# Performance work log

Measured on AMD Instinct MI355X. Metric: run time of the kernel, lower is better.

Reference implementation:

```python
import jax, jax.numpy as jnp
import numpy as np

N = 32768      # total points (multiple of patch_size -> no padding needed)
C = 768        # channels
H = 8          # num heads
K = 256        # patch_size (window length)
HD = C // H    # head dim = 96, divisible by 6 (3 axes * rotary pairs)
FREQ = 100.0   # rope_freq


def rope3d(x, pos):
    """Point-position RoPE: head dim split into 3 axis chunks, each rotated
    by angles pos_axis * freq**(-i/half).  x: [N,H,HD], pos: [N,3] float."""
    d_axis = HD // 3            # 32
    half = d_axis // 2          # 16
    inv_freq = FREQ ** (-jnp.arange(half, dtype=x.dtype) / half)   # [half]
    ang = pos[:, :, None] * inv_freq[None, None, :]                # [N,3,half]
    cos = jnp.cos(ang)[:, None, :, :]                              # [N,1,3,half]
    sin = jnp.sin(ang)[:, None, :, :]
    xr = x.reshape(x.shape[0], x.shape[1], 3, d_axis)              # [N,H,3,d_axis]
    x1, x2 = xr[..., :half], xr[..., half:]
    out = jnp.concatenate([x1 * cos - x2 * sin, x1 * sin + x2 * cos], axis=-1)
    return out.reshape(x.shape)


def setup_inputs() -> dict:
    key = jax.random.key(0)
    ks = jax.random.split(key, 6)
    feat = jax.random.normal(ks[0], (N, C), dtype=jnp.float32)
    grid_coord = jax.random.randint(ks[1], (N, 3), 0, 1024, dtype=jnp.int32)
    order = jax.random.permutation(ks[2], N).astype(jnp.int32)     # serialized order
    inverse = jnp.argsort(order).astype(jnp.int32)                 # its inverse
    w_qkv = jax.random.normal(ks[3], (C, 3 * C), dtype=jnp.float32) * 0.02
    b_qkv = jnp.zeros((3 * C,), dtype=jnp.float32)
    w_proj = jax.random.normal(ks[4], (C, C), dtype=jnp.float32) * 0.02
    b_proj = jnp.zeros((C,), dtype=jnp.float32)
    return {"feat": feat, "grid_coord": grid_coord, "order": order,
            "inverse": inverse, "w_qkv": w_qkv, "b_qkv": b_qkv,
            "w_proj": w_proj, "b_proj": b_proj}


def reference(feat, grid_coord, order, inverse, w_qkv, b_qkv, w_proj, b_proj):
    scale = HD ** -0.5
    P = N // K  # number of windows
    qkv = (feat @ w_qkv + b_qkv)[order]                   # gather by serialized order
    pos = grid_coord[order].astype(feat.dtype)            # [N,3]
    q, k, v = jnp.split(qkv, 3, axis=-1)
    q = rope3d(q.reshape(N, H, HD), pos)
    k = rope3d(k.reshape(N, H, HD), pos)
    v = v.reshape(N, H, HD)
    # windowed (varlen with equal patch lengths) attention
    qw = q.reshape(P, K, H, HD)
    kw = k.reshape(P, K, H, HD)
    vw = v.reshape(P, K, H, HD)
    logits = jnp.einsum('pqhd,pkhd->phqk', qw, kw) * scale
    attn = jax.nn.softmax(logits, axis=-1)
    out = jnp.einsum('phqk,pkhd->pqhd', attn, vw).reshape(N, C)
    out = out[inverse]                                    # scatter back to input order
    return out @ w_proj + b_proj
```

## Files before the change

kernel.cpp:

```cpp
#include <hip/hip_runtime.h>
#include <hip/hip_bf16.h>
#include <stdint.h>

typedef __bf16 bf16_t;
typedef __bf16 bf16x8 __attribute__((ext_vector_type(8)));
typedef __bf16 bf16x4 __attribute__((ext_vector_type(4)));
typedef float f32x4 __attribute__((ext_vector_type(4)));

template <int V> struct ic { static constexpr int value = V; };

__device__ __forceinline__ void gload_lds16(const bf16_t* g, bf16_t* l) {
  __builtin_amdgcn_global_load_lds((const __attribute__((address_space(1))) void*)g,
                                   (__attribute__((address_space(3))) void*)l, 16, 0, 0);
}

__global__ __launch_bounds__(256) void transpose_cast_k(const float* __restrict__ W,
                                                        bf16_t* __restrict__ Bt,
                                                        int KDin, int MDin) {
  __shared__ float tile[64][65];
  const int bm = blockIdx.x, bk = blockIdx.y;
  const int c = threadIdx.x & 63, r0 = threadIdx.x >> 6;
#pragma unroll
  for (int rr = 0; rr < 16; ++rr) {
    int row = rr * 4 + r0;
    tile[row][c] = W[(size_t)(bk * 64 + row) * MDin + bm * 64 + c];
  }
  __syncthreads();
#pragma unroll
  for (int rr = 0; rr < 16; ++rr) {
    int mo = rr * 4 + r0;
    Bt[(size_t)(bm * 64 + mo) * KDin + bk * 64 + c] = (bf16_t)tile[c][mo];
  }
}

__global__ __launch_bounds__(256) void gather_cast_k(const float* __restrict__ feat,
                                                     const int* __restrict__ order,
                                                     const int* __restrict__ grid_coord,
                                                     bf16_t* __restrict__ featp,
                                                     float* __restrict__ posf) {
  const int id = blockIdx.x * 256 + threadIdx.x;
  const int j = id / 192;
  const int c = (id % 192) * 4;
  const int g = order[j];
  const float4 v = *(const float4*)(feat + (size_t)g * 768 + c);
  bf16x4 o;
  o[0] = (bf16_t)v.x; o[1] = (bf16_t)v.y; o[2] = (bf16_t)v.z; o[3] = (bf16_t)v.w;
  *(bf16x4*)(featp + (size_t)j * 768 + c) = o;
  if (c == 0) {
    posf[j * 3 + 0] = (float)grid_coord[g * 3 + 0];
    posf[j * 3 + 1] = (float)grid_coord[g * 3 + 1];
    posf[j * 3 + 2] = (float)grid_coord[g * 3 + 2];
  }
}

template <int MODE, int NBX>
__global__ __launch_bounds__(512, 2) void gemm256_k(const bf16_t* __restrict__ A,
                                                    const bf16_t* __restrict__ Bt,
                                                    const float* __restrict__ bias,
                                                    bf16_t* __restrict__ Cq,
                                                    bf16_t* __restrict__ Ck,
                                                    bf16_t* __restrict__ Cv,
                                                    float* __restrict__ Cf,
                                                    const int* __restrict__ order,
                                                    const float* __restrict__ posf) {
  extern __shared__ bf16_t sm[];
  bf16_t* ldsA = sm;
  bf16_t* ldsB = sm + 4 * 8192;

  const int tid = threadIdx.x;
  const int lane = tid & 63, wave = tid >> 6;
  const int wr = wave >> 2, wc = wave & 3;
  const int lq = lane & 15, lk = lane >> 4;

  const int bid = blockIdx.x;
  const int cpx = gridDim.x >> 3;
  const int rm = (bid & 7) * cpx + (bid >> 3);
  const int by = rm / NBX, bx = rm % NBX;

  const int o0 = tid, o1 = tid + 512;
  const int r0s = o0 >> 2, ls0 = (o0 & 3) ^ ((r0s >> 1) & 3);
  const int r1s = o1 >> 2, ls1 = (o1 & 3) ^ ((r1s >> 1) & 3);
  const bf16_t* pA0 = A + (size_t)(by * 256 + r0s) * 768 + ls0 * 8;
  const bf16_t* pA1 = A + (size_t)(by * 256 + r1s) * 768 + ls1 * 8;
  const bf16_t* pB0 = Bt + (size_t)(bx * 256 + r0s) * 768 + ls0 * 8;
  const bf16_t* pB1 = Bt + (size_t)(bx * 256 + r1s) * 768 + ls1 * 8;

  auto stageA = [&](int kt) {
    bf16_t* d = ldsA + ((kt & 3) << 13);
    gload_lds16(pA0 + kt * 32, d + o0 * 8);
    gload_lds16(pA1 + kt * 32, d + o1 * 8);
  };
  auto stageB = [&](int kt) {
    bf16_t* d = ldsB + ((kt & 3) << 13);
    gload_lds16(pB0 + kt * 32, d + o0 * 8);
    gload_lds16(pB1 + kt * 32, d + o1 * 8);
  };

  const int pslot = lk ^ ((lq >> 1) & 3);

  f32x4 acc[8][4] = {};

  stageA(0); stageB(0); stageA(1); stageB(1); stageA(2); stageB(2);
  asm volatile("s_waitcnt vmcnt(8)" ::: "memory");
  __builtin_amdgcn_s_barrier();
  __builtin_amdgcn_sched_barrier(0);

  auto group = [&](int t, auto VMC, auto STGC) {
    constexpr int VM = decltype(VMC)::value;
    constexpr bool STG = decltype(STGC)::value;
    const bf16_t* Ab = ldsA + ((t & 3) << 13);
    const bf16_t* Bb = ldsB + ((t & 3) << 13);
    bf16x8 af[4], bfr[4];
#pragma unroll
    for (int m = 0; m < 4; ++m)
      af[m] = *(const bf16x8*)(Ab + (wr * 128 + m * 16 + lq) * 32 + pslot * 8);
#pragma unroll
    for (int n = 0; n < 4; ++n)
      bfr[n] = *(const bf16x8*)(Bb + (wc * 64 + n * 16 + lq) * 32 + pslot * 8);
    if constexpr (STG) stageA(t + 3);
    __builtin_amdgcn_s_barrier();
    asm volatile("s_waitcnt lgkmcnt(0)" ::: "memory");
    __builtin_amdgcn_s_setprio(1);
#pragma unroll
    for (int n = 0; n < 4; ++n)
#pragma unroll
      for (int m = 0; m < 4; ++m)
        acc[m][n] = __builtin_amdgcn_mfma_f32_16x16x32_bf16(af[m], bfr[n], acc[m][n], 0, 0, 0);
    __builtin_amdgcn_s_setprio(0);
    __builtin_amdgcn_s_barrier();
#pragma unroll
    for (int m = 0; m < 4; ++m)
      af[m] = *(const bf16x8*)(Ab + (wr * 128 + 64 + m * 16 + lq) * 32 + pslot * 8);
    if constexpr (STG) stageB(t + 3);
    if constexpr (VM == 8) asm volatile("s_waitcnt vmcnt(8)" ::: "memory");
    else if constexpr (VM == 4) asm volatile("s_waitcnt vmcnt(4)" ::: "memory");
    else if constexpr (VM == 0) asm volatile("s_waitcnt vmcnt(0)" ::: "memory");
    __builtin_amdgcn_s_barrier();
    asm volatile("s_waitcnt lgkmcnt(0)" ::: "memory");
    __builtin_amdgcn_s_setprio(1);
#pragma unroll
    for (int n = 0; n < 4; ++n)
#pragma unroll
      for (int m = 0; m < 4; ++m)
        acc[4 + m][n] = __builtin_amdgcn_mfma_f32_16x16x32_bf16(af[m], bfr[n], acc[4 + m][n], 0, 0, 0);
    __builtin_amdgcn_s_setprio(0);
    __builtin_amdgcn_s_barrier();
    __builtin_amdgcn_sched_barrier(0);
  };

  for (int t = 0; t < 21; ++t) group(t, ic<8>{}, ic<1>{});
  group(21, ic<4>{}, ic<0>{});
  group(22, ic<0>{}, ic<0>{});
  group(23, ic<-1>{}, ic<0>{});

  const int colb = bx * 256 + wc * 64;
  float bcol[4];
#pragma unroll
  for (int n = 0; n < 4; ++n) bcol[n] = bias[colb + n * 16 + lq];

  if (MODE == 0) {
    const int sec = bx / 3;
    bf16_t* base = sec == 0 ? Cq : (sec == 1 ? Ck : Cv);
    const int coll = colb - sec * 768;
    if (sec < 2) {
      const int a0 = (colb % 96) >> 5;
      const int a1 = ((colb + 32) % 96) >> 5;
      const float fr = exp2f(-0.41524101186f * (float)lq);
#pragma unroll
      for (int m = 0; m < 8; ++m) {
        const int rowb = by * 256 + wr * 128 + m * 16 + lk * 4;
#pragma unroll
        for (int r = 0; r < 4; ++r) {
          const int row = rowb + r;
          float s0, c0, s1, c1;
          __sincosf(posf[row * 3 + a0] * fr, &s0, &c0);
          __sincosf(posf[row * 3 + a1] * fr, &s1, &c1);
          const float x1 = acc[m][0][r] + bcol[0], x2 = acc[m][1][r] + bcol[1];
          const float y1 = acc[m][2][r] + bcol[2], y2 = acc[m][3][r] + bcol[3];
          acc[m][0][r] = x1 * c0 - x2 * s0;
          acc[m][1][r] = x1 * s0 + x2 * c0;
          acc[m][2][r] = y1 * c1 - y2 * s1;
          acc[m][3][r] = y1 * s1 + y2 * c1;
        }
#pragma unroll
        for (int n = 0; n < 4; ++n) {
          const int col = coll + n * 16 + lq;
#pragma unroll
          for (int r = 0; r < 4; ++r)
            base[(size_t)(rowb + r) * 768 + col] = (bf16_t)acc[m][n][r];
        }
      }
    } else {
#pragma unroll
      for (int m = 0; m < 8; ++m) {
        const int rowb = by * 256 + wr * 128 + m * 16 + lk * 4;
#pragma unroll
        for (int n = 0; n < 4; ++n) {
          const int col = coll + n * 16 + lq;
#pragma unroll
          for (int r = 0; r < 4; ++r)
            base[(size_t)(rowb + r) * 768 + col] = (bf16_t)(acc[m][n][r] + bcol[n]);
        }
      }
    }
  } else {
#pragma unroll
    for (int m = 0; m < 8; ++m) {
      const int rowb = by * 256 + wr * 128 + m * 16 + lk * 4;
      int ro[4];
#pragma unroll
      for (int r = 0; r < 4; ++r) ro[r] = order[rowb + r];
#pragma unroll
      for (int n = 0; n < 4; ++n) {
        const int col = colb + n * 16 + lq;
#pragma unroll
        for (int r = 0; r < 4; ++r)
          Cf[(size_t)ro[r] * 768 + col] = acc[m][n][r] + bcol[n];
      }
    }
  }
}

__global__ __launch_bounds__(256) void pack_k(const bf16_t* __restrict__ Kb,
                                              const bf16_t* __restrict__ Vb,
                                              bf16_t* __restrict__ Kp,
                                              bf16_t* __restrict__ Vp) {
  __shared__ bf16_t VT[96 * 264];
  const int h = blockIdx.x, p = blockIdx.y;
  const int tid = threadIdx.x;
  const int tok0 = p * 256;
  const size_t phb = (size_t)(p * 8 + h) * 24576;

#pragma unroll
  for (int i = 0; i < 12; ++i) {
    const int c = i * 256 + tid;
    const int fi = c >> 6, ln = c & 63;
    const int nt = fi / 3, a = fi - nt * 3;
    const int tok = nt * 16 + (ln & 15), feat = a * 32 + (ln >> 4) * 8;
    *(bf16x8*)(Kp + phb + (size_t)c * 8) =
        *(const bf16x8*)(Kb + (size_t)(tok0 + tok) * 768 + h * 96 + feat);
  }

  {
    const bf16_t* vrow = Vb + (size_t)(tok0 + tid) * 768 + h * 96;
#pragma unroll
    for (int d0 = 0; d0 < 96; d0 += 8) {
      bf16x8 v = *(const bf16x8*)(vrow + d0);
#pragma unroll
      for (int i = 0; i < 8; ++i) VT[(d0 + i) * 264 + tid] = v[i];
    }
  }
  __syncthreads();
#pragma unroll
  for (int i = 0; i < 12; ++i) {
    const int c = i * 256 + tid;
    const int fi = c >> 6, ln = c & 63;
    const int d = (fi >> 3) * 16 + (ln & 15);
    const int tb = (fi & 7) * 32 + (ln >> 4) * 8;
    *(bf16x8*)(Vp + phb + (size_t)c * 8) = *(const bf16x8*)(VT + d * 264 + tb);
  }
}

__global__ __launch_bounds__(256) void attn_k(bf16_t* QO,
                                              const bf16_t* __restrict__ Kp,
                                              const bf16_t* __restrict__ Vp) {
  __shared__ bf16_t KV[24576];
  __shared__ bf16_t Pb[4][2048];
  const int bid = blockIdx.x;
  const int chunk = bid & 3;
  const int ph = bid >> 2;
  const int h = ph & 7, p = ph >> 3;
  const int tid = threadIdx.x, lane = tid & 63, wave = tid >> 6;
  const int lq = lane & 15, lk = lane >> 4;
  const int tok0 = p * 256;
  const int qrow0 = chunk * 64 + wave * 16;
  const bf16_t* Kps = Kp + (size_t)ph * 24576;
  const bf16_t* Vps = Vp + (size_t)ph * 24576;
  const float scale = 0.10206207262f;

#pragma unroll
  for (int i = 0; i < 12; ++i)
    gload_lds16(Kps + i * 2048 + tid * 8, KV + i * 2048 + tid * 8);
  bf16x8 aq[3];
  {
    const bf16_t* qb = QO + (size_t)(tok0 + qrow0 + lq) * 768 + h * 96 + lk * 8;
#pragma unroll
    for (int kc = 0; kc < 3; ++kc) aq[kc] = *(const bf16x8*)(qb + kc * 32);
  }
  __syncthreads();

  f32x4 sacc[16];
#pragma unroll
  for (int nt = 0; nt < 16; ++nt) {
    f32x4 acc = {0.f, 0.f, 0.f, 0.f};
#pragma unroll
    for (int kc = 0; kc < 3; ++kc) {
      bf16x8 bk = *(const bf16x8*)(KV + (size_t)((nt * 3 + kc) * 64 + lane) * 8);
      acc = __builtin_amdgcn_mfma_f32_16x16x32_bf16(aq[kc], bk, acc, 0, 0, 0);
    }
    sacc[nt] = acc;
  }
  __syncthreads();

#pragma unroll
  for (int i = 0; i < 12; ++i)
    gload_lds16(Vps + i * 2048 + tid * 8, KV + i * 2048 + tid * 8);

  float linv[4];
#pragma unroll
  for (int r = 0; r < 4; ++r) {
    float mx = -1e30f;
#pragma unroll
    for (int nt = 0; nt < 16; ++nt) mx = fmaxf(mx, sacc[nt][r]);
    mx = fmaxf(mx, __shfl_xor(mx, 1));
    mx = fmaxf(mx, __shfl_xor(mx, 2));
    mx = fmaxf(mx, __shfl_xor(mx, 4));
    mx = fmaxf(mx, __shfl_xor(mx, 8));
    mx *= scale;
    float l = 0.f;
#pragma unroll
    for (int nt = 0; nt < 16; ++nt) {
      float e = __expf(sacc[nt][r] * scale - mx);
      sacc[nt][r] = e;
      l += e;
    }
    l += __shfl_xor(l, 1);
    l += __shfl_xor(l, 2);
    l += __shfl_xor(l, 4);
    l += __shfl_xor(l, 8);
    linv[r] = 1.f / l;
  }
  __syncthreads();

  bf16_t* pw = &Pb[wave][0];
  f32x4 oacc[6] = {};
#pragma unroll
  for (int hf = 0; hf < 2; ++hf) {
#pragma unroll
    for (int ntl = 0; ntl < 8; ++ntl) {
      const int nt = hf * 8 + ntl;
      const int chk = ntl * 2 + (lq >> 3);
#pragma unroll
      for (int r = 0; r < 4; ++r) {
        const int row = lk * 4 + r;
        const int phys = chk ^ (row & 7);
        pw[row * 128 + phys * 8 + (lq & 7)] = (bf16_t)sacc[nt][r];
      }
    }
#pragma unroll
    for (int kcl = 0; kcl < 4; ++kcl) {
      const int physr = (kcl * 4 + lk) ^ (lq & 7);
      bf16x8 pf = *(const bf16x8*)(pw + lq * 128 + physr * 8);
      const int kc = hf * 4 + kcl;
#pragma unroll
      for (int dt = 0; dt < 6; ++dt) {
        bf16x8 vb = *(const bf16x8*)(KV + (size_t)((dt * 8 + kc) * 64 + lane) * 8);
        oacc[dt] = __builtin_amdgcn_mfma_f32_16x16x32_bf16(pf, vb, oacc[dt], 0, 0, 0);
      }
    }
  }

#pragma unroll
  for (int dt = 0; dt < 6; ++dt) {
#pragma unroll
    for (int r = 0; r < 4; ++r) {
      const int row = tok0 + qrow0 + lk * 4 + r;
      QO[(size_t)row * 768 + h * 96 + dt * 16 + lq] = (bf16_t)(oacc[dt][r] * linv[r]);
    }
  }
}

extern "C" void kernel_launch(void* const* d_in, const int* in_sizes, int n_in,
                              void* d_out, int out_size, void* d_ws, size_t ws_size,
                              hipStream_t stream) {
  const float* feat       = (const float*)d_in[0];
  const int*   grid_coord = (const int*)d_in[1];
  const int*   order      = (const int*)d_in[2];
  const float* w_qkv      = (const float*)d_in[4];
  const float* b_qkv      = (const float*)d_in[5];
  const float* w_proj     = (const float*)d_in[6];
  const float* b_proj     = (const float*)d_in[7];
  float* out = (float*)d_out;

  char* ws = (char*)d_ws;
  bf16_t* Bt1   = (bf16_t*)(ws);
  bf16_t* Bt2   = (bf16_t*)(ws + 3538944);
  bf16_t* featp = (bf16_t*)(ws + 4718592);
  bf16_t* Kp    = featp;
  bf16_t* Qb    = (bf16_t*)(ws + 55050240);
  bf16_t* Kb    = (bf16_t*)(ws + 105381888);
  bf16_t* Vb    = (bf16_t*)(ws + 155713536);
  bf16_t* Vp    = (bf16_t*)(ws + 206045184);
  float*  posf  = (float*)(ws + 206045184);

  static bool attr_set = false;
  if (!attr_set) {
    (void)hipFuncSetAttribute((const void*)gemm256_k<0, 9>,
                              hipFuncAttributeMaxDynamicSharedMemorySize, 131072);
    (void)hipFuncSetAttribute((const void*)gemm256_k<1, 3>,
                              hipFuncAttributeMaxDynamicSharedMemorySize, 131072);
    attr_set = true;
  }

  transpose_cast_k<<<dim3(36, 12), 256, 0, stream>>>(w_qkv, Bt1, 768, 2304);
  transpose_cast_k<<<dim3(12, 12), 256, 0, stream>>>(w_proj, Bt2, 768, 768);
  gather_cast_k<<<24576, 256, 0, stream>>>(feat, order, grid_coord, featp, posf);
  gemm256_k<0, 9><<<1152, 512, 131072, stream>>>(featp, Bt1, b_qkv, Qb, Kb, Vb,
                                                 nullptr, nullptr, posf);
  pack_k<<<dim3(8, 128), 256, 0, stream>>>(Kb, Vb, Kp, Vp);
  attn_k<<<4096, 256, 0, stream>>>(Qb, Kp, Vp);
  gemm256_k<1, 3><<<384, 512, 131072, stream>>>(Qb, Bt2, b_proj, nullptr, nullptr,
                                                nullptr, out, order, nullptr);
}
```

Before: 502.8 us.

## Make GEMMs persistent over 128-row strips looping across all column tiles

Replaces the 256x256-tile GEMM grid with 256 blocks, each owning a 128-row strip of A and looping over every 256-wide column tile. The prefetch for the next tile's B is issued during the last k-steps of the current tile so the pipeline runs without draining. LDS use drops to 96KB and A is re-read from L2 per tile. The intent is to remove the tail-wave imbalance of 1152 and 384 tile launches on a 256-CU device and to overlap tile transitions. In exchange each block does a serial loop over 9 or 3 tiles, and the 128x256 tile has lower arithmetic intensity per LDS load.

```diff
diff --git a/kernel.cpp b/kernel.cpp
--- a/kernel.cpp
+++ b/kernel.cpp
@@ -53,8 +53,8 @@
   }
 }
 
-template <int MODE, int NBX>
-__global__ __launch_bounds__(512, 2) void gemm256_k(const bf16_t* __restrict__ A,
+template <int MODE, int NT>
+__global__ __launch_bounds__(512, 2) void gemm128_k(const bf16_t* __restrict__ A,
                                                     const bf16_t* __restrict__ Bt,
                                                     const float* __restrict__ bias,
                                                     bf16_t* __restrict__ Cq,
@@ -65,61 +65,56 @@
                                                     const float* __restrict__ posf) {
   extern __shared__ bf16_t sm[];
   bf16_t* ldsA = sm;
-  bf16_t* ldsB = sm + 4 * 8192;
+  bf16_t* ldsB = sm + 16384;
 
   const int tid = threadIdx.x;
   const int lane = tid & 63, wave = tid >> 6;
   const int wr = wave >> 2, wc = wave & 3;
   const int lq = lane & 15, lk = lane >> 4;
-
-  const int bid = blockIdx.x;
-  const int cpx = gridDim.x >> 3;
-  const int rm = (bid & 7) * cpx + (bid >> 3);
-  const int by = rm / NBX, bx = rm % NBX;
-
-  const int o0 = tid, o1 = tid + 512;
-  const int r0s = o0 >> 2, ls0 = (o0 & 3) ^ ((r0s >> 1) & 3);
-  const int r1s = o1 >> 2, ls1 = (o1 & 3) ^ ((r1s >> 1) & 3);
-  const bf16_t* pA0 = A + (size_t)(by * 256 + r0s) * 768 + ls0 * 8;
-  const bf16_t* pA1 = A + (size_t)(by * 256 + r1s) * 768 + ls1 * 8;
-  const bf16_t* pB0 = Bt + (size_t)(bx * 256 + r0s) * 768 + ls0 * 8;
-  const bf16_t* pB1 = Bt + (size_t)(bx * 256 + r1s) * 768 + ls1 * 8;
-
-  auto stageA = [&](int kt) {
-    bf16_t* d = ldsA + ((kt & 3) << 13);
-    gload_lds16(pA0 + kt * 32, d + o0 * 8);
-    gload_lds16(pA1 + kt * 32, d + o1 * 8);
+  const int by = blockIdx.x;
+
+  const int oA = tid;
+  const int rA = oA >> 2, lsA = (oA & 3) ^ ((rA >> 1) & 3);
+  const int oB0 = tid, oB1 = tid + 512;
+  const int rB0 = oB0 >> 2, lsB0 = (oB0 & 3) ^ ((rB0 >> 1) & 3);
+  const int rB1 = oB1 >> 2, lsB1 = (oB1 & 3) ^ ((rB1 >> 1) & 3);
+
+  const bf16_t* pA = A + (size_t)(by * 128 + rA) * 768 + lsA * 8;
+  const bf16_t* pB0 = Bt + (size_t)rB0 * 768 + lsB0 * 8;
+  const bf16_t* pB1 = Bt + (size_t)rB1 * 768 + lsB1 * 8;
+
+  auto stage = [&](const bf16_t* sB0, const bf16_t* sB1, int kt, int slot) {
+    bf16_t* dA = ldsA + (slot << 12);
+    bf16_t* dB = ldsB + (slot << 13);
+    gload_lds16(pA + kt * 32, dA + oA * 8);
+    gload_lds16(sB0 + kt * 32, dB + oB0 * 8);
+    gload_lds16(sB1 + kt * 32, dB + oB1 * 8);
   };
-  auto stageB = [&](int kt) {
-    bf16_t* d = ldsB + ((kt & 3) << 13);
-    gload_lds16(pB0 + kt * 32, d + o0 * 8);
-    gload_lds16(pB1 + kt * 32, d + o1 * 8);
-  };
 
   const int pslot = lk ^ ((lq >> 1) & 3);
 
-  f32x4 acc[8][4] = {};
-
-  stageA(0); stageB(0); stageA(1); stageB(1); stageA(2); stageB(2);
-  asm volatile("s_waitcnt vmcnt(8)" ::: "memory");
-  __builtin_amdgcn_s_barrier();
-  __builtin_amdgcn_sched_barrier(0);
-
-  auto group = [&](int t, auto VMC, auto STGC) {
+  f32x4 acc[4][4];
+
+  auto ph = [&](int t, const bf16_t* sB0, const bf16_t* sB1, int skt,
+                auto VMC, auto STGC) {
     constexpr int VM = decltype(VMC)::value;
     constexpr bool STG = decltype(STGC)::value;
-    const bf16_t* Ab = ldsA + ((t & 3) << 13);
+    const bf16_t* Ab = ldsA + ((t & 3) << 12);
     const bf16_t* Bb = ldsB + ((t & 3) << 13);
     bf16x8 af[4], bfr[4];
 #pragma unroll
     for (int m = 0; m < 4; ++m)
-      af[m] = *(const bf16x8*)(Ab + (wr * 128 + m * 16 + lq) * 32 + pslot * 8);
+      af[m] = *(const bf16x8*)(Ab + (wr * 64 + m * 16 + lq) * 32 + pslot * 8);
 #pragma unroll
     for (int n = 0; n < 4; ++n)
       bfr[n] = *(const bf16x8*)(Bb + (wc * 64 + n * 16 + lq) * 32 + pslot * 8);
-    if constexpr (STG) stageA(t + 3);
+    if constexpr (STG) stage(sB0, sB1, skt, (t + 3) & 3);
+    if constexpr (VM == 6) asm volatile("s_waitcnt vmcnt(6)" ::: "memory");
+    else if constexpr (VM == 3) asm volatile("s_waitcnt vmcnt(3)" ::: "memory");
+    else if constexpr (VM == 0) asm volatile("s_waitcnt vmcnt(0)" ::: "memory");
     __builtin_amdgcn_s_barrier();
     asm volatile("s_waitcnt lgkmcnt(0)" ::: "memory");
+    __builtin_amdgcn_sched_barrier(0);
     __builtin_amdgcn_s_setprio(1);
 #pragma unroll
     for (int n = 0; n < 4; ++n)
@@ -128,96 +123,106 @@
         acc[m][n] = __builtin_amdgcn_mfma_f32_16x16x32_bf16(af[m], bfr[n], acc[m][n], 0, 0, 0);
     __builtin_amdgcn_s_setprio(0);
     __builtin_amdgcn_s_barrier();
-#pragma unroll
-    for (int m = 0; m < 4; ++m)
-      af[m] = *(const bf16x8*)(Ab + (wr * 128 + 64 + m * 16 + lq) * 32 + pslot * 8);
-    if constexpr (STG) stageB(t + 3);
-    if constexpr (VM == 8) asm volatile("s_waitcnt vmcnt(8)" ::: "memory");
-    else if constexpr (VM == 4) asm volatile("s_waitcnt vmcnt(4)" ::: "memory");
-    else if constexpr (VM == 0) asm volatile("s_waitcnt vmcnt(0)" ::: "memory");
-    __builtin_amdgcn_s_barrier();
-    asm volatile("s_waitcnt lgkmcnt(0)" ::: "memory");
-    __builtin_amdgcn_s_setprio(1);
-#pragma unroll
-    for (int n = 0; n < 4; ++n)
-#pragma unroll
-      for (int m = 0; m < 4; ++m)
-        acc[4 + m][n] = __builtin_amdgcn_mfma_f32_16x16x32_bf16(af[m], bfr[n], acc[4 + m][n], 0, 0, 0);
-    __builtin_amdgcn_s_setprio(0);
-    __builtin_amdgcn_s_barrier();
     __builtin_amdgcn_sched_barrier(0);
   };
 
-  for (int t = 0; t < 21; ++t) group(t, ic<8>{}, ic<1>{});
-  group(21, ic<4>{}, ic<0>{});
-  group(22, ic<0>{}, ic<0>{});
-  group(23, ic<-1>{}, ic<0>{});
-
-  const int colb = bx * 256 + wc * 64;
-  float bcol[4];
-#pragma unroll
-  for (int n = 0; n < 4; ++n) bcol[n] = bias[colb + n * 16 + lq];
-
-  if (MODE == 0) {
-    const int sec = bx / 3;
-    bf16_t* base = sec == 0 ? Cq : (sec == 1 ? Ck : Cv);
-    const int coll = colb - sec * 768;
-    if (sec < 2) {
-      const int a0 = (colb % 96) >> 5;
-      const int a1 = ((colb + 32) % 96) >> 5;
-      const float fr = exp2f(-0.41524101186f * (float)lq);
-#pragma unroll
-      for (int m = 0; m < 8; ++m) {
-        const int rowb = by * 256 + wr * 128 + m * 16 + lk * 4;
-#pragma unroll
-        for (int r = 0; r < 4; ++r) {
-          const int row = rowb + r;
-          float s0, c0, s1, c1;
-          __sincosf(posf[row * 3 + a0] * fr, &s0, &c0);
-          __sincosf(posf[row * 3 + a1] * fr, &s1, &c1);
-          const float x1 = acc[m][0][r] + bcol[0], x2 = acc[m][1][r] + bcol[1];
-          const float y1 = acc[m][2][r] + bcol[2], y2 = acc[m][3][r] + bcol[3];
-          acc[m][0][r] = x1 * c0 - x2 * s0;
-          acc[m][1][r] = x1 * s0 + x2 * c0;
-          acc[m][2][r] = y1 * c1 - y2 * s1;
-          acc[m][3][r] = y1 * s1 + y2 * c1;
+  stage(pB0, pB1, 0, 0);
+  stage(pB0, pB1, 1, 1);
+  stage(pB0, pB1, 2, 2);
+  asm volatile("s_waitcnt vmcnt(6)" ::: "memory");
+  __builtin_amdgcn_s_barrier();
+  __builtin_amdgcn_sched_barrier(0);
+
+  for (int tile = 0; tile < NT; ++tile) {
+#pragma unroll
+    for (int m = 0; m < 4; ++m)
+#pragma unroll
+      for (int n = 0; n < 4; ++n) acc[m][n] = f32x4{0.f, 0.f, 0.f, 0.f};
+
+    const bf16_t* nB0 = pB0 + 256 * 768;
+    const bf16_t* nB1 = pB1 + 256 * 768;
+
+    for (int t = 0; t < 21; ++t) ph(t, pB0, pB1, t + 3, ic<6>{}, ic<1>{});
+    if (tile < NT - 1) {
+      ph(21, nB0, nB1, 0, ic<6>{}, ic<1>{});
+      ph(22, nB0, nB1, 1, ic<6>{}, ic<1>{});
+      ph(23, nB0, nB1, 2, ic<6>{}, ic<1>{});
+    } else {
+      ph(21, nB0, nB1, 0, ic<3>{}, ic<0>{});
+      ph(22, nB0, nB1, 1, ic<0>{}, ic<0>{});
+      ph(23, nB0, nB1, 2, ic<-1>{}, ic<0>{});
+    }
+
+    const int bx = tile;
+    const int colb = bx * 256 + wc * 64;
+    float bcol[4];
+#pragma unroll
+    for (int n = 0; n < 4; ++n) bcol[n] = bias[colb + n * 16 + lq];
+
+    if (MODE == 0) {
+      const int sec = bx / 3;
+      bf16_t* base = sec == 0 ? Cq : (sec == 1 ? Ck : Cv);
+      const int coll = colb - sec * 768;
+      if (sec < 2) {
+        const int a0 = (colb % 96) >> 5;
+        const int a1 = ((colb + 32) % 96) >> 5;
+        const float fr = exp2f(-0.41524101186f * (float)lq);
+#pragma unroll
+        for (int m = 0; m < 4; ++m) {
+          const int rowb = by * 128 + wr * 64 + m * 16 + lk * 4;
+#pragma unroll
+          for (int r = 0; r < 4; ++r) {
+            const int row = rowb + r;
+            float s0, c0, s1, c1;
+            __sincosf(posf[row * 3 + a0] * fr, &s0, &c0);
+            __sincosf(posf[row * 3 + a1] * fr, &s1, &c1);
+            const float x1 = acc[m][0][r] + bcol[0], x2 = acc[m][1][r] + bcol[1];
+            const float y1 = acc[m][2][r] + bcol[2], y2 = acc[m][3][r] + bcol[3];
+            acc[m][0][r] = x1 * c0 - x2 * s0;
+            acc[m][1][r] = x1 * s0 + x2 * c0;
+            acc[m][2][r] = y1 * c1 - y2 * s1;
+            acc[m][3][r] = y1 * s1 + y2 * c1;
+          }
+#pragma unroll
+          for (int n = 0; n < 4; ++n) {
+            const int col = coll + n * 16 + lq;
+#pragma unroll
+            for (int r = 0; r < 4; ++r)
+              base[(size_t)(rowb + r) * 768 + col] = (bf16_t)acc[m][n][r];
+          }
         }
-#pragma unroll
-        for (int n = 0; n < 4; ++n) {
-          const int col = coll + n * 16 + lq;
-#pragma unroll
-          for (int r = 0; r < 4; ++r)
-            base[(size_t)(rowb + r) * 768 + col] = (bf16_t)acc[m][n][r];
+      } else {
+#pragma unroll
+        for (int m = 0; m < 4; ++m) {
+          const int rowb = by * 128 + wr * 64 + m * 16 + lk * 4;
+#pragma unroll
+          for (int n = 0; n < 4; ++n) {
+            const int col = coll + n * 16 + lq;
+#pragma unroll
+            for (int r = 0; r < 4; ++r)
+              base[(size_t)(rowb + r) * 768 + col] = (bf16_t)(acc[m][n][r] + bcol[n]);
+          }
         }
       }
     } else {
 #pragma unroll
-      for (int m = 0; m < 8; ++m) {
-        const int rowb = by * 256 + wr * 128 + m * 16 + lk * 4;
+      for (int m = 0; m < 4; ++m) {
+        const int rowb = by * 128 + wr * 64 + m * 16 + lk * 4;
+        int ro[4];
+#pragma unroll
+        for (int r = 0; r < 4; ++r) ro[r] = order[rowb + r];
 #pragma unroll
         for (int n = 0; n < 4; ++n) {
-          const int col = coll + n * 16 + lq;
+          const int col = colb + n * 16 + lq;
 #pragma unroll
           for (int r = 0; r < 4; ++r)
-            base[(size_t)(rowb + r) * 768 + col] = (bf16_t)(acc[m][n][r] + bcol[n]);
+            Cf[(size_t)ro[r] * 768 + col] = acc[m][n][r] + bcol[n];
         }
       }
     }
-  } else {
-#pragma unroll
-    for (int m = 0; m < 8; ++m) {
-      const int rowb = by * 256 + wr * 128 + m * 16 + lk * 4;
-      int ro[4];
-#pragma unroll
-      for (int r = 0; r < 4; ++r) ro[r] = order[rowb + r];
-#pragma unroll
-      for (int n = 0; n < 4; ++n) {
-        const int col = colb + n * 16 + lq;
-#pragma unroll
-        for (int r = 0; r < 4; ++r)
-          Cf[(size_t)ro[r] * 768 + col] = acc[m][n][r] + bcol[n];
-      }
-    }
+
+    pB0 = nB0;
+    pB1 = nB1;
   }
 }
 
@@ -395,20 +400,20 @@
 
   static bool attr_set = false;
   if (!attr_set) {
-    (void)hipFuncSetAttribute((const void*)gemm256_k<0, 9>,
-                              hipFuncAttributeMaxDynamicSharedMemorySize, 131072);
-    (void)hipFuncSetAttribute((const void*)gemm256_k<1, 3>,
-                              hipFuncAttributeMaxDynamicSharedMemorySize, 131072);
+    (void)hipFuncSetAttribute((const void*)gemm128_k<0, 9>,
+                              hipFuncAttributeMaxDynamicSharedMemorySize, 98304);
+    (void)hipFuncSetAttribute((const void*)gemm128_k<1, 3>,
+                              hipFuncAttributeMaxDynamicSharedMemorySize, 98304);
     attr_set = true;
   }
 
   transpose_cast_k<<<dim3(36, 12), 256, 0, stream>>>(w_qkv, Bt1, 768, 2304);
   transpose_cast_k<<<dim3(12, 12), 256, 0, stream>>>(w_proj, Bt2, 768, 768);
   gather_cast_k<<<24576, 256, 0, stream>>>(feat, order, grid_coord, featp, posf);
-  gemm256_k<0, 9><<<1152, 512, 131072, stream>>>(featp, Bt1, b_qkv, Qb, Kb, Vb,
-                                                 nullptr, nullptr, posf);
+  gemm128_k<0, 9><<<256, 512, 98304, stream>>>(featp, Bt1, b_qkv, Qb, Kb, Vb,
+                                               nullptr, nullptr, posf);
   pack_k<<<dim3(8, 128), 256, 0, stream>>>(Kb, Vb, Kp, Vp);
   attn_k<<<4096, 256, 0, stream>>>(Qb, Kp, Vp);
-  gemm256_k<1, 3><<<384, 512, 131072, stream>>>(Qb, Bt2, b_proj, nullptr, nullptr,
-                                                nullptr, out, order, nullptr);
-}
+  gemm128_k<1, 3><<<256, 512, 98304, stream>>>(Qb, Bt2, b_proj, nullptr, nullptr,
+                                               nullptr, out, order, nullptr);
+}
```

Result: slower. 568.3 us (+13.0%).

## Drop pack kernel: write V transposed from GEMM, gather K directly in attention

Applied to the files above, without the earlier changes.

The QKV GEMM epilogue now writes V in transposed [channel][token] layout using 4-wide bf16 stores. The attention kernel gathers K tiles straight from row-major Kb and V tiles from the transposed buffer through global-to-LDS loads, so the separate pack kernel and its extra read/write pass over K and V are removed. In exchange, the V stores in the GEMM epilogue are strided across rows of 32768 tokens, and the attention loads become less contiguous than the pre-packed layout.

```diff
diff --git a/kernel.cpp b/kernel.cpp
--- a/kernel.cpp
+++ b/kernel.cpp
@@ -160,9 +160,9 @@
 
   if (MODE == 0) {
     const int sec = bx / 3;
-    bf16_t* base = sec == 0 ? Cq : (sec == 1 ? Ck : Cv);
     const int coll = colb - sec * 768;
     if (sec < 2) {
+      bf16_t* base = sec == 0 ? Cq : Ck;
       const int a0 = (colb % 96) >> 5;
       const int a1 = ((colb + 32) % 96) >> 5;
       const float fr = exp2f(-0.41524101186f * (float)lq);
@@ -197,9 +197,10 @@
 #pragma unroll
         for (int n = 0; n < 4; ++n) {
           const int col = coll + n * 16 + lq;
-#pragma unroll
-          for (int r = 0; r < 4; ++r)
-            base[(size_t)(rowb + r) * 768 + col] = (bf16_t)(acc[m][n][r] + bcol[n]);
+          bf16x4 o;
+#pragma unroll
+          for (int r = 0; r < 4; ++r) o[r] = (bf16_t)(acc[m][n][r] + bcol[n]);
+          *(bf16x4*)(Cv + (size_t)col * 32768 + rowb) = o;
         }
       }
     }
@@ -221,49 +222,9 @@
   }
 }
 
-__global__ __launch_bounds__(256) void pack_k(const bf16_t* __restrict__ Kb,
-                                              const bf16_t* __restrict__ Vb,
-                                              bf16_t* __restrict__ Kp,
-                                              bf16_t* __restrict__ Vp) {
-  __shared__ bf16_t VT[96 * 264];
-  const int h = blockIdx.x, p = blockIdx.y;
-  const int tid = threadIdx.x;
-  const int tok0 = p * 256;
-  const size_t phb = (size_t)(p * 8 + h) * 24576;
-
-#pragma unroll
-  for (int i = 0; i < 12; ++i) {
-    const int c = i * 256 + tid;
-    const int fi = c >> 6, ln = c & 63;
-    const int nt = fi / 3, a = fi - nt * 3;
-    const int tok = nt * 16 + (ln & 15), feat = a * 32 + (ln >> 4) * 8;
-    *(bf16x8*)(Kp + phb + (size_t)c * 8) =
-        *(const bf16x8*)(Kb + (size_t)(tok0 + tok) * 768 + h * 96 + feat);
-  }
-
-  {
-    const bf16_t* vrow = Vb + (size_t)(tok0 + tid) * 768 + h * 96;
-#pragma unroll
-    for (int d0 = 0; d0 < 96; d0 += 8) {
-      bf16x8 v = *(const bf16x8*)(vrow + d0);
-#pragma unroll
-      for (int i = 0; i < 8; ++i) VT[(d0 + i) * 264 + tid] = v[i];
-    }
-  }
-  __syncthreads();
-#pragma unroll
-  for (int i = 0; i < 12; ++i) {
-    const int c = i * 256 + tid;
-    const int fi = c >> 6, ln = c & 63;
-    const int d = (fi >> 3) * 16 + (ln & 15);
-    const int tb = (fi & 7) * 32 + (ln >> 4) * 8;
-    *(bf16x8*)(Vp + phb + (size_t)c * 8) = *(const bf16x8*)(VT + d * 264 + tb);
-  }
-}
-
 __global__ __launch_bounds__(256) void attn_k(bf16_t* QO,
-                                              const bf16_t* __restrict__ Kp,
-                                              const bf16_t* __restrict__ Vp) {
+                                              const bf16_t* __restrict__ Kb,
+                                              const bf16_t* __restrict__ Vt) {
   __shared__ bf16_t KV[24576];
   __shared__ bf16_t Pb[4][2048];
   const int bid = blockIdx.x;
@@ -274,13 +235,16 @@
   const int lq = lane & 15, lk = lane >> 4;
   const int tok0 = p * 256;
   const int qrow0 = chunk * 64 + wave * 16;
-  const bf16_t* Kps = Kp + (size_t)ph * 24576;
-  const bf16_t* Vps = Vp + (size_t)ph * 24576;
   const float scale = 0.10206207262f;
 
 #pragma unroll
-  for (int i = 0; i < 12; ++i)
-    gload_lds16(Kps + i * 2048 + tid * 8, KV + i * 2048 + tid * 8);
+  for (int i = 0; i < 12; ++i) {
+    const int fi = i * 4 + wave;
+    const int nt = fi / 3, a = fi - nt * 3;
+    const bf16_t* src = Kb + (size_t)(tok0 + nt * 16 + (lane & 15)) * 768 +
+                        h * 96 + a * 32 + (lane >> 4) * 8;
+    gload_lds16(src, KV + i * 2048 + tid * 8);
+  }
   bf16x8 aq[3];
   {
     const bf16_t* qb = QO + (size_t)(tok0 + qrow0 + lq) * 768 + h * 96 + lk * 8;
@@ -303,8 +267,13 @@
   __syncthreads();
 
 #pragma unroll
-  for (int i = 0; i < 12; ++i)
-    gload_lds16(Vps + i * 2048 + tid * 8, KV + i * 2048 + tid * 8);
+  for (int i = 0; i < 12; ++i) {
+    const int fi = i * 4 + wave;
+    const int d = (fi >> 3) * 16 + (lane & 15);
+    const int tb = (fi & 7) * 32 + (lane >> 4) * 8;
+    const bf16_t* src = Vt + (size_t)(h * 96 + d) * 32768 + tok0 + tb;
+    gload_lds16(src, KV + i * 2048 + tid * 8);
+  }
 
   float linv[4];
 #pragma unroll
@@ -386,11 +355,9 @@
   bf16_t* Bt1   = (bf16_t*)(ws);
   bf16_t* Bt2   = (bf16_t*)(ws + 3538944);
   bf16_t* featp = (bf16_t*)(ws + 4718592);
-  bf16_t* Kp    = featp;
   bf16_t* Qb    = (bf16_t*)(ws + 55050240);
   bf16_t* Kb    = (bf16_t*)(ws + 105381888);
-  bf16_t* Vb    = (bf16_t*)(ws + 155713536);
-  bf16_t* Vp    = (bf16_t*)(ws + 206045184);
+  bf16_t* Vt    = (bf16_t*)(ws + 155713536);
   float*  posf  = (float*)(ws + 206045184);
 
   static bool attr_set = false;
@@ -405,10 +372,9 @@
   transpose_cast_k<<<dim3(36, 12), 256, 0, stream>>>(w_qkv, Bt1, 768, 2304);
   transpose_cast_k<<<dim3(12, 12), 256, 0, stream>>>(w_proj, Bt2, 768, 768);
   gather_cast_k<<<24576, 256, 0, stream>>>(feat, order, grid_coord, featp, posf);
-  gemm256_k<0, 9><<<1152, 512, 131072, stream>>>(featp, Bt1, b_qkv, Qb, Kb, Vb,
+  gemm256_k<0, 9><<<1152, 512, 131072, stream>>>(featp, Bt1, b_qkv, Qb, Kb, Vt,
                                                  nullptr, nullptr, posf);
-  pack_k<<<dim3(8, 128), 256, 0, stream>>>(Kb, Vb, Kp, Vp);
-  attn_k<<<4096, 256, 0, stream>>>(Qb, Kp, Vp);
+  attn_k<<<4096, 256, 0, stream>>>(Qb, Kb, Vt);
   gemm256_k<1, 3><<<384, 512, 131072, stream>>>(Qb, Bt2, b_proj, nullptr, nullptr,
                                                 nullptr, out, order, nullptr);
 }
```

Result: faster. 483.7 us (-3.8%).
